# Optimization experiments

Hardware: AMD Instinct MI355X
Metric: run time of the kernel (lower is better)

Reference implementation:

```python
import jax, jax.numpy as jnp
import numpy as np

H = 384  # LSTM hidden size


def _conv1d(x, w, b, stride):
    # x: [B, T, Cin], w: [K, Cin, Cout] (flax 'SAME' padding, channels-last)
    y = jax.lax.conv_general_dilated(
        x, w, window_strides=(stride,), padding='SAME',
        dimension_numbers=('NWC', 'WIO', 'NWC'))
    return y + b


def _lstm(x, Wi, Wh, b, reverse):
    # x: [B, T, D]; Wi: [D, 4H] (input proj, no bias in flax LSTMCell input dense),
    # Wh: [H, 4H] (recurrent proj), b: [4H]. Gate order: i, f, g, o.
    if reverse:
        x = x[:, ::-1]
    B = x.shape[0]
    # precompute all input-to-gate projections in one big GEMM: [B, T, 4H]
    xg = jnp.einsum('btd,dh->bth', x, Wi)

    def step(carry, xg_t):
        c, h = carry
        z = xg_t + h @ Wh + b                      # [B, 4H]
        i, f, g, o = jnp.split(z, 4, axis=-1)
        i = jax.nn.sigmoid(i)
        f = jax.nn.sigmoid(f)
        g = jnp.tanh(g)
        o = jax.nn.sigmoid(o)
        c = f * c + i * g
        h = o * jnp.tanh(c)
        return (c, h), h

    init = (jnp.zeros((B, H), x.dtype), jnp.zeros((B, H), x.dtype))
    _, hs = jax.lax.scan(step, init, jnp.swapaxes(xg, 0, 1))  # hs: [T, B, H]
    hs = jnp.swapaxes(hs, 0, 1)
    if reverse:  # keep_order=True: flip output back to original time order
        hs = hs[:, ::-1]
    return hs


def setup_inputs() -> dict:
    key = jax.random.key(0)
    ks = jax.random.split(key, 12)
    s = 0.05
    B, T = 128, 8000
    return {
        'x': jax.random.normal(ks[0], (B, T, 1), jnp.float32),
        'conv1_w': jax.random.normal(ks[1], (5, 1, 4), jnp.float32) * s,
        'conv1_b': jnp.zeros((4,), jnp.float32),
        'conv2_w': jax.random.normal(ks[2], (5, 4, 16), jnp.float32) * s,
        'conv2_b': jnp.zeros((16,), jnp.float32),
        'conv3_w': jax.random.normal(ks[3], (19, 16, H), jnp.float32) * s,
        'conv3_b': jnp.zeros((H,), jnp.float32),
        'lstm_Wi': jax.random.normal(ks[4], (5, H, 4 * H), jnp.float32) * s,
        'lstm_Wh': jax.random.normal(ks[5], (5, H, 4 * H), jnp.float32) * s,
        'lstm_b': jnp.zeros((5, 4 * H), jnp.float32),
        'dense_w': jax.random.normal(ks[6], (H, 5), jnp.float32) * s,
        'dense_b': jnp.zeros((5,), jnp.float32),
    }


def reference(x, conv1_w, conv1_b, conv2_w, conv2_b, conv3_w, conv3_b,
              lstm_Wi, lstm_Wh, lstm_b, dense_w, dense_b):
    # CNN feature extractor
    x = jax.nn.silu(_conv1d(x, conv1_w, conv1_b, 1))
    x = jax.nn.silu(_conv1d(x, conv2_w, conv2_b, 1))
    x = jax.nn.silu(_conv1d(x, conv3_w, conv3_b, 5))   # [B, T/5, 384]
    # 5 stacked LSTMs, layers 1,3,5 reversed (keep_order), layers 2,4 forward
    for i in range(5):
        x = _lstm(x, lstm_Wi[i], lstm_Wh[i], lstm_b[i], reverse=(i % 2 == 0))
    # CTC head
    return x @ dense_w + dense_b                       # [B, T/5, 5]
```

## Files before the change

### kernel.cpp

```cpp
#include <hip/hip_runtime.h>
#include <math.h>

#define B_SZ 128
#define T_IN 8000
#define T_OUT 1600
#define HDIM 384
#define GDIM 1536
#define TC 40
#define NCHUNK (T_OUT / TC)
#define NTILES (12 * (B_SZ * TC / 128))
#define NLB 64

typedef _Float16 f16;
typedef __attribute__((ext_vector_type(2))) _Float16 f16x2;
typedef __attribute__((ext_vector_type(4))) _Float16 f16x4;
typedef __attribute__((ext_vector_type(8))) _Float16 f16x8;
typedef __attribute__((ext_vector_type(4))) float f32x4;
typedef __attribute__((ext_vector_type(4))) unsigned int u32x4;

__device__ inline float fdot2(f16x2 a, f16x2 b, float c) {
#if __has_builtin(__builtin_amdgcn_fdot2)
  return __builtin_amdgcn_fdot2(a, b, c, false);
#else
  return fmaf((float)a[0], (float)b[0], fmaf((float)a[1], (float)b[1], c));
#endif
}

__device__ inline float rcp_fast(float x) {
#if __has_builtin(__builtin_amdgcn_rcpf)
  return __builtin_amdgcn_rcpf(x);
#else
  return 1.f / x;
#endif
}
__device__ inline float sigf(float z) { return rcp_fast(1.f + __expf(-z)); }
__device__ inline float tanh_fast(float z) {
  z = fminf(fmaxf(z, -15.f), 15.f);
  float e = __expf(2.f * z);
  return (e - 1.f) * rcp_fast(e + 1.f);
}

__global__ __launch_bounds__(256) void conv12_kernel(
    const float* __restrict__ x, const float* __restrict__ w1, const float* __restrict__ b1,
    const float* __restrict__ w2, const float* __restrict__ b2, f16* __restrict__ y2) {
  __shared__ float sw1[20], sb1[4], sw2[320], sb2[16];
  int tid = threadIdx.x;
  if (tid < 20) sw1[tid] = w1[tid];
  if (tid < 4)  sb1[tid] = b1[tid];
  if (tid < 16) sb2[tid] = b2[tid];
  for (int i = tid; i < 320; i += 256) sw2[i] = w2[i];
  __syncthreads();
  int flat = blockIdx.x * 256 + tid;
  int b = flat / T_IN, t = flat % T_IN;
  const float* xb = x + (size_t)b * T_IN;
  float xv[9];
#pragma unroll
  for (int d = 0; d < 9; ++d) {
    int tt = t + d - 4;
    xv[d] = (tt >= 0 && tt < T_IN) ? xb[tt] : 0.f;
  }
  float y1[5][4];
#pragma unroll
  for (int u = 0; u < 5; ++u) {
    int tau = t + u - 2;
    bool valid = (tau >= 0 && tau < T_IN);
#pragma unroll
    for (int co = 0; co < 4; ++co) {
      float a = sb1[co];
#pragma unroll
      for (int k = 0; k < 5; ++k) a = fmaf(xv[u + k], sw1[k * 4 + co], a);
      y1[u][co] = valid ? (a / (1.f + expf(-a))) : 0.f;
    }
  }
  f16x8 o0, o1;
#pragma unroll
  for (int co = 0; co < 16; ++co) {
    float a = sb2[co];
#pragma unroll
    for (int u = 0; u < 5; ++u)
#pragma unroll
      for (int ci = 0; ci < 4; ++ci)
        a = fmaf(y1[u][ci], sw2[(u * 4 + ci) * 16 + co], a);
    float sv = a / (1.f + expf(-a));
    if (co < 8) o0[co] = (f16)sv; else o1[co - 8] = (f16)sv;
  }
  f16x8* dst = (f16x8*)(y2 + (size_t)flat * 16);
  dst[0] = o0;
  dst[1] = o1;
}

__global__ __launch_bounds__(256) void w3cvt_kernel(
    const float* __restrict__ w3, f16* __restrict__ w3t) {
  int idx = blockIdx.x * 256 + threadIdx.x;
  int c = idx / 320, k = idx - c * 320;
  w3t[idx] = (k < 304) ? (f16)w3[(size_t)k * 384 + c] : (f16)0.f;
}

#define C3M 32
#define C3K 320
#define INSP 24
#define BSTP 40

__global__ __launch_bounds__(384) void conv3_kernel(
    const f16* __restrict__ y2, const f16* __restrict__ w3t,
    const float* __restrict__ b3, f16* __restrict__ act) {
  __shared__ f16 in_s[176 * INSP];
  __shared__ f16 bs_t[384 * BSTP];
  int tid = threadIdx.x;
  int b = blockIdx.y;
  int t0 = blockIdx.x * C3M;
  int base_t = t0 * 5 - 7;
  for (int j = tid; j < 352; j += 384) {
    int tau = j >> 1, ci0 = (j & 1) * 8;
    int tt = base_t + tau;
    f16x8 v = {};
    if (tt >= 0 && tt < T_IN)
      v = *(const f16x8*)(y2 + ((size_t)b * T_IN + tt) * 16 + ci0);
    *(f16x8*)&in_s[tau * INSP + ci0] = v;
  }
  int wv = tid >> 6;
  int l = tid & 63;
  int lm = l & 15;
  int lk = l >> 4;
  f32x4 acc[2][4];
#pragma unroll
  for (int mt = 0; mt < 2; ++mt)
#pragma unroll
    for (int q = 0; q < 4; ++q) acc[mt][q] = (f32x4){0.f, 0.f, 0.f, 0.f};
  for (int ks = 0; ks < 10; ++ks) {
    __syncthreads();
    for (int u = tid; u < 1536; u += 384) {
      int c = u >> 2, k8 = u & 3;
      *(f16x8*)&bs_t[c * BSTP + k8 * 8] =
          *(const f16x8*)(w3t + (size_t)c * C3K + ks * 32 + k8 * 8);
    }
    __syncthreads();
    int kg = ks * 32 + lk * 8;
    int kk = kg >> 4, ci = kg & 15;
    f16x8 a0 = *(const f16x8*)&in_s[(lm * 5 + kk) * INSP + ci];
    f16x8 a1 = *(const f16x8*)&in_s[((lm + 16) * 5 + kk) * INSP + ci];
#pragma unroll
    for (int q = 0; q < 4; ++q) {
      f16x8 bf = *(const f16x8*)&bs_t[((wv * 4 + q) * 16 + lm) * BSTP + lk * 8];
      acc[0][q] = __builtin_amdgcn_mfma_f32_16x16x32_f16(a0, bf, acc[0][q], 0, 0, 0);
      acc[1][q] = __builtin_amdgcn_mfma_f32_16x16x32_f16(a1, bf, acc[1][q], 0, 0, 0);
    }
  }
#pragma unroll
  for (int mt = 0; mt < 2; ++mt)
#pragma unroll
    for (int q = 0; q < 4; ++q) {
      int n = (wv * 4 + q) * 16 + lm;
      float bv = b3[n];
#pragma unroll
      for (int r = 0; r < 4; ++r) {
        int m = mt * 16 + lk * 4 + r;
        float a = acc[mt][q][r] + bv;
        a = a / (1.f + expf(-a));
        act[((size_t)b * T_OUT + t0 + m) * HDIM + n] = (f16)a;
      }
    }
}

__global__ __launch_bounds__(256) void whcvt_kernel(
    const float* __restrict__ Wh, f16x2* __restrict__ whB) {
  size_t idx = (size_t)blockIdx.x * 256 + threadIdx.x;
  int d = (int)(idx & 3);
  size_t r1 = idx >> 2;
  int lane = (int)(r1 & 63);
  size_t r2 = r1 >> 6;
  int ks = (int)(r2 % 12);
  size_t r3 = r2 / 12;
  int nt = (int)(r3 % 12);
  size_t r4 = r3 / 12;
  int isl = (int)(r4 & 7);
  int L = (int)(r4 >> 3);
  int cz = nt * 16 + (lane & 15);
  int gate = cz & 3;
  int jj = cz >> 2;
  int gcol = gate * 384 + isl * 48 + jj;
  int k2d = ks * 16 + (lane >> 4) * 4 + d;
  const float* src = Wh + ((size_t)L * 384 + 2 * k2d) * 1536 + gcol;
  f16x2 v;
  v[0] = (f16)src[0];
  v[1] = (f16)src[1536];
  whB[idx] = v;
}

__global__ __launch_bounds__(256) void gemm_xg_kernel(
    const f16* __restrict__ act, const float* __restrict__ Bw,
    f16* __restrict__ C, int lo) {
  __shared__ f16x2 As2[8 * 136];
  __shared__ f16x2 Bs2[8 * 128];
  int tid = threadIdx.x;
  int n0 = blockIdx.x * 128;
  int m0 = blockIdx.y * 128;
  int am = tid >> 2;
  int ak = (tid & 3) * 4;
  int bk = tid >> 5;
  int bn = (tid & 31) * 4;
  int row0 = m0 + am, row1 = row0 + 64;
  const f16* Ap0 = act + ((size_t)(row0 / TC) * T_OUT + lo + row0 % TC) * HDIM + ak;
  const f16* Ap1 = act + ((size_t)(row1 / TC) * T_OUT + lo + row1 % TC) * HDIM + ak;
  const float* Bp = Bw + (size_t)(2 * bk) * GDIM + n0 + bn;
  f16x4 ra0 = *(const f16x4*)Ap0;
  f16x4 ra1 = *(const f16x4*)Ap1;
  float4 rb0 = *(const float4*)Bp;
  float4 rb1 = *(const float4*)(Bp + (size_t)GDIM);
  float acc[8][8];
#pragma unroll
  for (int i = 0; i < 8; ++i)
#pragma unroll
    for (int j = 0; j < 8; ++j) acc[i][j] = 0.f;
  int tx = tid & 15, ty = tid >> 4;
  for (int kt = 0; kt < 24; ++kt) {
    int ak2 = ak >> 1;
    As2[(ak2 + 0) * 136 + am] = (f16x2){ra0[0], ra0[1]};
    As2[(ak2 + 1) * 136 + am] = (f16x2){ra0[2], ra0[3]};
    As2[(ak2 + 0) * 136 + am + 64] = (f16x2){ra1[0], ra1[1]};
    As2[(ak2 + 1) * 136 + am + 64] = (f16x2){ra1[2], ra1[3]};
    Bs2[bk * 128 + bn + 0] = (f16x2){(f16)rb0.x, (f16)rb1.x};
    Bs2[bk * 128 + bn + 1] = (f16x2){(f16)rb0.y, (f16)rb1.y};
    Bs2[bk * 128 + bn + 2] = (f16x2){(f16)rb0.z, (f16)rb1.z};
    Bs2[bk * 128 + bn + 3] = (f16x2){(f16)rb0.w, (f16)rb1.w};
    __syncthreads();
    if (kt < 23) {
      Ap0 += 16; Ap1 += 16; Bp += (size_t)16 * GDIM;
      ra0 = *(const f16x4*)Ap0;
      ra1 = *(const f16x4*)Ap1;
      rb0 = *(const float4*)Bp;
      rb1 = *(const float4*)(Bp + (size_t)GDIM);
    }
#pragma unroll
    for (int k2 = 0; k2 < 8; ++k2) {
      f16x8 a0 = *(const f16x8*)&As2[k2 * 136 + ty * 4];
      f16x8 a1 = *(const f16x8*)&As2[k2 * 136 + 64 + ty * 4];
      f16x8 b0 = *(const f16x8*)&Bs2[k2 * 128 + tx * 4];
      f16x8 b1 = *(const f16x8*)&Bs2[k2 * 128 + 64 + tx * 4];
      f16x2 av[8], bv[8];
#pragma unroll
      for (int q = 0; q < 4; ++q) {
        av[q] = (f16x2){a0[2 * q], a0[2 * q + 1]};
        av[q + 4] = (f16x2){a1[2 * q], a1[2 * q + 1]};
        bv[q] = (f16x2){b0[2 * q], b0[2 * q + 1]};
        bv[q + 4] = (f16x2){b1[2 * q], b1[2 * q + 1]};
      }
#pragma unroll
      for (int i = 0; i < 8; ++i)
#pragma unroll
        for (int j = 0; j < 8; ++j) acc[i][j] = fdot2(av[i], bv[j], acc[i][j]);
    }
    __syncthreads();
  }
#pragma unroll
  for (int i = 0; i < 8; ++i) {
    int mi = (i < 4) ? (ty * 4 + i) : (64 + ty * 4 + i - 4);
    f16* Cp = C + (size_t)(m0 + mi) * GDIM + n0;
    f16x4 p0, p1;
    p0[0] = (f16)acc[i][0]; p0[1] = (f16)acc[i][1]; p0[2] = (f16)acc[i][2]; p0[3] = (f16)acc[i][3];
    p1[0] = (f16)acc[i][4]; p1[1] = (f16)acc[i][5]; p1[2] = (f16)acc[i][6]; p1[3] = (f16)acc[i][7];
    *(f16x4*)(Cp + tx * 4) = p0;
    *(f16x4*)(Cp + 64 + tx * 4) = p1;
  }
}

#define HSTR 784

union FusedSh {
  struct { char h2s[16 * HSTR]; unsigned pub[16 * 25]; } L;
  struct { f16x2 As2[3][8 * 136]; f16x2 Bs2[3][8 * 128]; } G;
  char pad[25600];
};

__global__ __launch_bounds__(768, 1) void fused_kernel(
    const f16* __restrict__ xgc_rd, f16* __restrict__ xgc_wr,
    const f16* __restrict__ whB, const float* __restrict__ bias,
    f16* __restrict__ act, float* __restrict__ cst, const float* __restrict__ Wi,
    unsigned* __restrict__ xh,
    int lo_l, int lo_g, int reverse, int first, int do_gemm, int epoch) {
  __shared__ FusedSh sh;
  int tid = threadIdx.x;

  if (blockIdx.x < NLB) {
    int wid = blockIdx.x;
    int g = wid & 7;
    int isl = wid >> 3;
    int b0 = g * 16;
    int nt = tid >> 6;
    int l = tid & 63;
    int bg = l >> 4;
    int qj = (l >> 2) & 3;
    int gate = l & 3;
    int jj = nt * 4 + qj;
    int hcol = isl * 48 + jj;
    int gcol = gate * 384 + isl * 48 + jj;

    f16x8 wreg[12];
    {
      const f16x8* wp = (const f16x8*)whB + (size_t)(isl * 12 + nt) * 12 * 64 + l;
#pragma unroll
      for (int ks = 0; ks < 12; ++ks) wreg[ks] = wp[(size_t)ks * 64];
#pragma unroll
      for (int ks = 0; ks < 12; ++ks) asm volatile("" : "+v"(wreg[ks]));
    }
    float bias_own = bias[gcol];

    float c_reg[4];
    if (first) {
#pragma unroll
      for (int r = 0; r < 4; ++r) c_reg[r] = 0.f;
      for (int i = tid; i < 16 * HSTR / 16; i += 768)
        *(f16x8*)(sh.L.h2s + i * 16) = (f16x8){};
    } else {
      int tprev = reverse ? (lo_l + TC) : (lo_l - 1);
#pragma unroll
      for (int r = 0; r < 4; ++r)
        c_reg[r] = cst[(size_t)(b0 + bg * 4 + r) * HDIM + hcol];
      int flat = tid * 8;
      int bt = flat / 384, c0 = flat % 384;
      *(f16x8*)(sh.L.h2s + bt * HSTR + c0 * 2) =
          *(const f16x8*)(act + ((size_t)(b0 + bt) * T_OUT + tprev) * HDIM + c0);
    }
    __syncthreads();

    const char* arow = sh.L.h2s + (l & 15) * HSTR + (l >> 4) * 16;
    unsigned short* pubh = (unsigned short*)sh.L.pub;

    int k2 = (tid % 3 == 0) ? (768 + tid / 3) : -1;

    float xv[4];
    {
      int tl0 = reverse ? (TC - 1) : 0;
      const f16* xb = xgc_rd + ((size_t)(b0 + bg * 4) * TC + tl0) * GDIM + gcol;
#pragma unroll
      for (int r = 0; r < 4; ++r) xv[r] = (float)xb[(size_t)r * TC * GDIM];
    }

    for (int s = 0; s < TC; ++s) {
      int t = reverse ? (lo_l + TC - 1 - s) : (lo_l + s);

      f32x4 acc = {0.f, 0.f, 0.f, 0.f};
#pragma unroll
      for (int ks = 0; ks < 12; ++ks) {
        f16x8 a = *(const f16x8*)(arow + ks * 64);
        acc = __builtin_amdgcn_mfma_f32_16x16x32_f16(a, wreg[ks], acc, 0, 0, 0);
      }

      f16 h16[4];
#pragma unroll
      for (int r = 0; r < 4; ++r) {
        float a = acc[r] + xv[r] + bias_own;
        float b = __shfl_xor(a, 1);
        float cc = __shfl_xor(a, 2);
        float dd = __shfl_xor(b, 2);
        float zi = (gate == 0) ? a : (gate == 1) ? b : (gate == 2) ? cc : dd;
        float zf = (gate == 1) ? a : (gate == 0) ? b : (gate == 3) ? cc : dd;
        float zg = (gate == 2) ? a : (gate == 3) ? b : (gate == 0) ? cc : dd;
        float zo = (gate == 3) ? a : (gate == 2) ? b : (gate == 1) ? cc : dd;
        float ig = sigf(zi), fg = sigf(zf), gv = tanh_fast(zg), og = sigf(zo);
        c_reg[r] = fg * c_reg[r] + ig * gv;
        h16[r] = (f16)(og * tanh_fast(c_reg[r]));
      }

      if (s + 1 < TC) {
        unsigned tag = (unsigned)(epoch * TC + s + 1);
        unsigned* slotbase = xh + (size_t)(s & 1) * 128 * 256;

        if (gate == 0) {
          int lcol = nt * 4 + qj;
#pragma unroll
          for (int r = 0; r < 4; ++r)
            pubh[(bg * 4 + r) * 50 + lcol] = __builtin_bit_cast(unsigned short, h16[r]);
        }
        __syncthreads();

        if (tid < 128) {
          int bt = tid >> 3, u = tid & 7;
          const unsigned* pw = sh.L.pub + bt * 25 + u * 3;
          u32x4 dnew;
          dnew[0] = pw[0]; dnew[1] = pw[1]; dnew[2] = pw[2]; dnew[3] = tag;
          u32x4* dp = (u32x4*)(slotbase + (((size_t)(b0 + bt) * 64) + isl * 8 + u) * 4);
          asm volatile("global_store_dwordx4 %0, %1, off sc0 sc1"
                       :: "v"(dp), "v"(dnew) : "memory");
        }

        if (gate == 0) {
#pragma unroll
          for (int r = 0; r < 4; ++r)
            act[((size_t)(b0 + bg * 4 + r) * T_OUT + t) * HDIM + hcol] = h16[r];
        }
        {
          int tl_n = reverse ? (TC - 2 - s) : (s + 1);
          const f16* xb = xgc_rd + ((size_t)(b0 + bg * 4) * TC + tl_n) * GDIM + gcol;
#pragma unroll
          for (int r = 0; r < 4; ++r) xv[r] = (float)xb[(size_t)r * TC * GDIM];
        }

        const u32x4* upA = nullptr; const u32x4* upB = nullptr;
        unsigned* dstA = nullptr; unsigned* dstB = nullptr;
#pragma unroll
        for (int uu = 0; uu < 2; ++uu) {
          int k = (uu == 0) ? tid : k2;
          if (uu == 1 && k < 0) break;
          int bt = k >> 6, rem = k & 63;
          int isl_src = rem >> 3, u = rem & 7;
          unsigned* dst = (unsigned*)(sh.L.h2s + bt * HSTR + isl_src * 96 + u * 12);
          if (isl_src == isl) {
            const unsigned* pw = sh.L.pub + bt * 25 + u * 3;
            dst[0] = pw[0]; dst[1] = pw[1]; dst[2] = pw[2];
          } else {
            const u32x4* up = (const u32x4*)(slotbase + (((size_t)(b0 + bt) * 64) + rem) * 4);
            if (!upA) { upA = up; dstA = dst; } else { upB = up; dstB = dst; }
          }
        }
        if (upA && !upB) {
          u32x4 v;
          while (true) {
            asm volatile("global_load_dwordx4 %0, %1, off sc0 sc1\n\ts_waitcnt vmcnt(0)"
                         : "=v"(v) : "v"(upA) : "memory");
            if (v[3] >= tag) break;
            __builtin_amdgcn_s_sleep(1);
          }
          dstA[0] = v[0]; dstA[1] = v[1]; dstA[2] = v[2];
        } else if (upA && upB) {
          u32x4 v0, v1;
          while (true) {
            asm volatile("global_load_dwordx4 %0, %2, off sc0 sc1\n\t"
                         "global_load_dwordx4 %1, %3, off sc0 sc1\n\t"
                         "s_waitcnt vmcnt(0)"
                         : "=&v"(v0), "=&v"(v1) : "v"(upA), "v"(upB) : "memory");
            if (v0[3] >= tag && v1[3] >= tag) break;
            __builtin_amdgcn_s_sleep(1);
          }
          dstA[0] = v0[0]; dstA[1] = v0[1]; dstA[2] = v0[2];
          dstB[0] = v1[0]; dstB[1] = v1[1]; dstB[2] = v1[2];
        }
        __syncthreads();
      } else {
        if (gate == 0) {
#pragma unroll
          for (int r = 0; r < 4; ++r)
            act[((size_t)(b0 + bg * 4 + r) * T_OUT + t) * HDIM + hcol] = h16[r];
        }
      }
    }
    if (gate == 0) {
#pragma unroll
      for (int r = 0; r < 4; ++r)
        cst[(size_t)(b0 + bg * 4 + r) * HDIM + hcol] = c_reg[r];
    }
  } else {
    if (!do_gemm) return;
    int wid = blockIdx.x - NLB;
    int sub = tid >> 8;
    int stid = tid & 255;
    int tileid = wid + 192 * sub;
    bool valid = (tileid < NTILES);
    int tclamp = valid ? tileid : 0;
    int n0 = (tclamp % 12) * 128;
    int m0 = (tclamp / 12) * 128;
    f16x2* As2 = &sh.G.As2[sub][0];
    f16x2* Bs2 = &sh.G.Bs2[sub][0];
    int am = stid >> 2;
    int ak = (stid & 3) * 4;
    int bk = stid >> 5;
    int bn = (stid & 31) * 4;
    int row0 = m0 + am, row1 = row0 + 64;
    const f16* Ap0 = act + ((size_t)(row0 / TC) * T_OUT + lo_g + row0 % TC) * HDIM + ak;
    const f16* Ap1 = act + ((size_t)(row1 / TC) * T_OUT + lo_g + row1 % TC) * HDIM + ak;
    const float* Bp = Wi + (size_t)(2 * bk) * GDIM + n0 + bn;
    f16x4 ra0 = {}, ra1 = {};
    float4 rb0 = {}, rb1 = {};
    if (valid) {
      ra0 = *(const f16x4*)Ap0;
      ra1 = *(const f16x4*)Ap1;
      rb0 = *(const float4*)Bp;
      rb1 = *(const float4*)(Bp + (size_t)GDIM);
    }
    float acc[8][8];
#pragma unroll
    for (int i = 0; i < 8; ++i)
#pragma unroll
      for (int j = 0; j < 8; ++j) acc[i][j] = 0.f;
    int tx = stid & 15, ty = stid >> 4;
    for (int kt = 0; kt < 24; ++kt) {
      if (valid) {
        int ak2 = ak >> 1;
        As2[(ak2 + 0) * 136 + am] = (f16x2){ra0[0], ra0[1]};
        As2[(ak2 + 1) * 136 + am] = (f16x2){ra0[2], ra0[3]};
        As2[(ak2 + 0) * 136 + am + 64] = (f16x2){ra1[0], ra1[1]};
        As2[(ak2 + 1) * 136 + am + 64] = (f16x2){ra1[2], ra1[3]};
        Bs2[bk * 128 + bn + 0] = (f16x2){(f16)rb0.x, (f16)rb1.x};
        Bs2[bk * 128 + bn + 1] = (f16x2){(f16)rb0.y, (f16)rb1.y};
        Bs2[bk * 128 + bn + 2] = (f16x2){(f16)rb0.z, (f16)rb1.z};
        Bs2[bk * 128 + bn + 3] = (f16x2){(f16)rb0.w, (f16)rb1.w};
      }
      __syncthreads();
      if (valid) {
        if (kt < 23) {
          Ap0 += 16; Ap1 += 16; Bp += (size_t)16 * GDIM;
          ra0 = *(const f16x4*)Ap0;
          ra1 = *(const f16x4*)Ap1;
          rb0 = *(const float4*)Bp;
          rb1 = *(const float4*)(Bp + (size_t)GDIM);
        }
#pragma unroll
        for (int k2i = 0; k2i < 8; ++k2i) {
          f16x8 a0 = *(const f16x8*)&As2[k2i * 136 + ty * 4];
          f16x8 a1 = *(const f16x8*)&As2[k2i * 136 + 64 + ty * 4];
          f16x8 b0 = *(const f16x8*)&Bs2[k2i * 128 + tx * 4];
          f16x8 b1 = *(const f16x8*)&Bs2[k2i * 128 + 64 + tx * 4];
          f16x2 av[8], bv[8];
#pragma unroll
          for (int qq = 0; qq < 4; ++qq) {
            av[qq] = (f16x2){a0[2 * qq], a0[2 * qq + 1]};
            av[qq + 4] = (f16x2){a1[2 * qq], a1[2 * qq + 1]};
            bv[qq] = (f16x2){b0[2 * qq], b0[2 * qq + 1]};
            bv[qq + 4] = (f16x2){b1[2 * qq], b1[2 * qq + 1]};
          }
#pragma unroll
          for (int i = 0; i < 8; ++i)
#pragma unroll
            for (int j = 0; j < 8; ++j) acc[i][j] = fdot2(av[i], bv[j], acc[i][j]);
        }
      }
      __syncthreads();
    }
    if (valid) {
#pragma unroll
      for (int i = 0; i < 8; ++i) {
        int mi = (i < 4) ? (ty * 4 + i) : (64 + ty * 4 + i - 4);
        f16* Cp = xgc_wr + (size_t)(m0 + mi) * GDIM + n0;
        f16x4 p0, p1;
        p0[0] = (f16)acc[i][0]; p0[1] = (f16)acc[i][1]; p0[2] = (f16)acc[i][2]; p0[3] = (f16)acc[i][3];
        p1[0] = (f16)acc[i][4]; p1[1] = (f16)acc[i][5]; p1[2] = (f16)acc[i][6]; p1[3] = (f16)acc[i][7];
        *(f16x4*)(Cp + tx * 4) = p0;
        *(f16x4*)(Cp + 64 + tx * 4) = p1;
      }
    }
  }
}

__global__ __launch_bounds__(256) void dense_kernel(
    const f16* __restrict__ h, const float* __restrict__ dw,
    const float* __restrict__ db, float* __restrict__ out) {
  __shared__ float ws_[1920];
  __shared__ float bs[5];
  int tid = threadIdx.x;
  for (int i = tid; i < 1920; i += 256) ws_[i] = dw[i];
  if (tid < 5) bs[tid] = db[tid];
  __syncthreads();
  size_t flat = (size_t)blockIdx.x * 256 + tid;
  const f16* hp = h + flat * HDIM;
  float acc[5];
#pragma unroll
  for (int o = 0; o < 5; ++o) acc[o] = bs[o];
  for (int d = 0; d < HDIM; d += 4) {
    f16x4 hv = *(const f16x4*)(hp + d);
#pragma unroll
    for (int o = 0; o < 5; ++o) {
      acc[o] = fmaf((float)hv[0], ws_[(d + 0) * 5 + o], acc[o]);
      acc[o] = fmaf((float)hv[1], ws_[(d + 1) * 5 + o], acc[o]);
      acc[o] = fmaf((float)hv[2], ws_[(d + 2) * 5 + o], acc[o]);
      acc[o] = fmaf((float)hv[3], ws_[(d + 3) * 5 + o], acc[o]);
    }
  }
  float* op = out + flat * 5;
#pragma unroll
  for (int o = 0; o < 5; ++o) op[o] = acc[o];
}

extern "C" void kernel_launch(void* const* d_in, const int* in_sizes, int n_in,
                              void* d_out, int out_size, void* d_ws, size_t ws_size,
                              hipStream_t stream) {
  const float* x  = (const float*)d_in[0];
  const float* w1 = (const float*)d_in[1];
  const float* b1 = (const float*)d_in[2];
  const float* w2 = (const float*)d_in[3];
  const float* b2 = (const float*)d_in[4];
  const float* w3 = (const float*)d_in[5];
  const float* b3 = (const float*)d_in[6];
  const float* Wi = (const float*)d_in[7];
  const float* Wh = (const float*)d_in[8];
  const float* lb = (const float*)d_in[9];
  const float* dw = (const float*)d_in[10];
  const float* db = (const float*)d_in[11];
  float* out = (float*)d_out;
  char* ws = (char*)d_ws;

  const size_t ACT_BYTES = (size_t)B_SZ * T_OUT * HDIM * 2;
  const size_t XGC_BYTES = (size_t)B_SZ * TC * GDIM * 2;
  const size_t WHB_BYTES = (size_t)5 * 8 * 12 * 12 * 64 * 16;
  const size_t CST_BYTES = (size_t)B_SZ * HDIM * 4;
  const size_t XH_BYTES  = (size_t)2 * 128 * 64 * 16;
  const size_t W3T_BYTES = (size_t)384 * 320 * 2;
  f16*      act  = (f16*)ws;
  f16*      xgcA = (f16*)(ws + ACT_BYTES);
  f16*      xgcB = (f16*)(ws + ACT_BYTES + XGC_BYTES);
  f16*      whB  = (f16*)(ws + ACT_BYTES + 2 * XGC_BYTES);
  float*    cst  = (float*)(ws + ACT_BYTES + 2 * XGC_BYTES + WHB_BYTES);
  unsigned* xh   = (unsigned*)(ws + ACT_BYTES + 2 * XGC_BYTES + WHB_BYTES + CST_BYTES);
  f16*      w3t  = (f16*)(ws + ACT_BYTES + 2 * XGC_BYTES + WHB_BYTES + CST_BYTES + XH_BYTES);
  f16* y2 = xgcA;

  hipMemsetAsync(xh, 0, XH_BYTES, stream);

  hipLaunchKernelGGL(conv12_kernel, dim3(B_SZ * T_IN / 256), dim3(256), 0, stream,
                     x, w1, b1, w2, b2, y2);
  hipLaunchKernelGGL(w3cvt_kernel, dim3(384 * 320 / 256), dim3(256), 0, stream,
                     w3, w3t);
  hipLaunchKernelGGL(conv3_kernel, dim3(T_OUT / C3M, B_SZ), dim3(384), 0, stream,
                     y2, w3t, b3, act);
  hipLaunchKernelGGL(whcvt_kernel, dim3((unsigned)(WHB_BYTES / 4 / 256)), dim3(256), 0, stream,
                     Wh, (f16x2*)whB);

  for (int l = 0; l < 5; ++l) {
    int rev = (l % 2 == 0) ? 1 : 0;
    const float* wi_p = Wi + (size_t)l * HDIM * GDIM;
    const f16* wh_p = whB + (size_t)l * 8 * 12 * 12 * 64 * 8;
    const float* lb_p = lb + (size_t)l * GDIM;
    int lo0 = rev ? (T_OUT - TC) : 0;
    hipLaunchKernelGGL(gemm_xg_kernel, dim3(GDIM / 128, (B_SZ * TC) / 128), dim3(256), 0, stream,
                       act, wi_p, xgcA, lo0);
    for (int ci = 0; ci < NCHUNK; ++ci) {
      int lo_l = rev ? (T_OUT - (ci + 1) * TC) : (ci * TC);
      int do_gemm = (ci + 1 < NCHUNK) ? 1 : 0;
      int lo_g = do_gemm ? (rev ? (T_OUT - (ci + 2) * TC) : ((ci + 1) * TC)) : 0;
      f16* rd = (ci % 2 == 0) ? xgcA : xgcB;
      f16* wr = (ci % 2 == 0) ? xgcB : xgcA;
      int epoch = l * NCHUNK + ci;
      hipLaunchKernelGGL(fused_kernel, dim3(256), dim3(768), 0, stream,
                         rd, wr, wh_p, lb_p, act, cst, wi_p, xh,
                         lo_l, lo_g, rev, (ci == 0) ? 1 : 0, do_gemm, epoch);
    }
  }
  hipLaunchKernelGGL(dense_kernel, dim3((B_SZ * T_OUT) / 256), dim3(256), 0, stream,
                     act, dw, db, out);
}
```

Before: 26.47 ms.

## Repartition LSTM recurrent blocks into 16 batch groups by 4 hidden slices

```diff
diff --git a/kernel.cpp b/kernel.cpp
--- a/kernel.cpp
+++ b/kernel.cpp
@@ -171,14 +171,14 @@
   size_t r2 = r1 >> 6;
   int ks = (int)(r2 % 12);
   size_t r3 = r2 / 12;
-  int nt = (int)(r3 % 12);
-  size_t r4 = r3 / 12;
-  int isl = (int)(r4 & 7);
-  int L = (int)(r4 >> 3);
+  int nt = (int)(r3 % 24);
+  size_t r4 = r3 / 24;
+  int isl = (int)(r4 & 3);
+  int L = (int)(r4 >> 2);
   int cz = nt * 16 + (lane & 15);
   int gate = cz & 3;
   int jj = cz >> 2;
-  int gcol = gate * 384 + isl * 48 + jj;
+  int gcol = gate * 384 + isl * 96 + jj;
   int k2d = ks * 16 + (lane >> 4) * 4 + d;
   const float* src = Wh + ((size_t)L * 384 + 2 * k2d) * 1536 + gcol;
   f16x2 v;
@@ -283,171 +283,193 @@
 
   if (blockIdx.x < NLB) {
     int wid = blockIdx.x;
-    int g = wid & 7;
-    int isl = wid >> 3;
-    int b0 = g * 16;
-    int nt = tid >> 6;
+    int g = wid & 15;
+    int isl = wid >> 4;
+    int b0 = g * 8;
+    int w = tid >> 6;
     int l = tid & 63;
-    int bg = l >> 4;
+    int lk = l >> 4;
     int qj = (l >> 2) & 3;
     int gate = l & 3;
-    int jj = nt * 4 + qj;
-    int hcol = isl * 48 + jj;
-    int gcol = gate * 384 + isl * 48 + jj;
-
-    f16x8 wreg[12];
+    int jj0 = w * 8 + qj;
+    int hcol0 = isl * 96 + jj0;
+    int gcol0 = gate * 384 + hcol0;
+    int bq = (lk & 1) * 4;
+
+    f16x8 wreg[2][12];
     {
-      const f16x8* wp = (const f16x8*)whB + (size_t)(isl * 12 + nt) * 12 * 64 + l;
-#pragma unroll
-      for (int ks = 0; ks < 12; ++ks) wreg[ks] = wp[(size_t)ks * 64];
-#pragma unroll
-      for (int ks = 0; ks < 12; ++ks) asm volatile("" : "+v"(wreg[ks]));
-    }
-    float bias_own = bias[gcol];
-
-    float c_reg[4];
+      const f16x8* wp = (const f16x8*)whB + (size_t)(isl * 24 + 2 * w) * 12 * 64 + l;
+#pragma unroll
+      for (int ks = 0; ks < 12; ++ks) {
+        wreg[0][ks] = wp[(size_t)ks * 64];
+        wreg[1][ks] = wp[(size_t)(12 + ks) * 64];
+      }
+#pragma unroll
+      for (int ks = 0; ks < 12; ++ks) {
+        asm volatile("" : "+v"(wreg[0][ks]));
+        asm volatile("" : "+v"(wreg[1][ks]));
+      }
+    }
+    float bias0 = bias[gcol0];
+    float bias1 = bias[gcol0 + 4];
+
+    float c0[4], c1[4];
     if (first) {
 #pragma unroll
-      for (int r = 0; r < 4; ++r) c_reg[r] = 0.f;
-      for (int i = tid; i < 16 * HSTR / 16; i += 768)
+      for (int r = 0; r < 4; ++r) { c0[r] = 0.f; c1[r] = 0.f; }
+      for (int i = tid; i < 784; i += 768)
         *(f16x8*)(sh.L.h2s + i * 16) = (f16x8){};
     } else {
       int tprev = reverse ? (lo_l + TC) : (lo_l - 1);
 #pragma unroll
-      for (int r = 0; r < 4; ++r)
-        c_reg[r] = cst[(size_t)(b0 + bg * 4 + r) * HDIM + hcol];
-      int flat = tid * 8;
-      int bt = flat / 384, c0 = flat % 384;
-      *(f16x8*)(sh.L.h2s + bt * HSTR + c0 * 2) =
-          *(const f16x8*)(act + ((size_t)(b0 + bt) * T_OUT + tprev) * HDIM + c0);
+      for (int r = 0; r < 4; ++r) {
+        c0[r] = cst[(size_t)(b0 + bq + r) * HDIM + hcol0];
+        c1[r] = cst[(size_t)(b0 + bq + r) * HDIM + hcol0 + 4];
+      }
+      int flat = tid * 4;
+      int bt = flat / 384, cc0 = flat % 384;
+      *(f16x4*)(sh.L.h2s + bt * HSTR + cc0 * 2) =
+          *(const f16x4*)(act + ((size_t)(b0 + bt) * T_OUT + tprev) * HDIM + cc0);
+      if (tid < 392) {
+        int row = 8 + tid / 49, off = (tid % 49) * 16;
+        *(f16x8*)(sh.L.h2s + row * HSTR + off) = (f16x8){};
+      }
     }
     __syncthreads();
 
-    const char* arow = sh.L.h2s + (l & 15) * HSTR + (l >> 4) * 16;
+    const char* arow = sh.L.h2s + (l & 15) * HSTR + lk * 16;
     unsigned short* pubh = (unsigned short*)sh.L.pub;
 
-    int k2 = (tid % 3 == 0) ? (768 + tid / 3) : -1;
-
-    float xv[4];
+    float xv0[4], xv1[4];
     {
       int tl0 = reverse ? (TC - 1) : 0;
-      const f16* xb = xgc_rd + ((size_t)(b0 + bg * 4) * TC + tl0) * GDIM + gcol;
-#pragma unroll
-      for (int r = 0; r < 4; ++r) xv[r] = (float)xb[(size_t)r * TC * GDIM];
+      const f16* xb = xgc_rd + ((size_t)(b0 + bq) * TC + tl0) * GDIM + gcol0;
+#pragma unroll
+      for (int r = 0; r < 4; ++r) {
+        xv0[r] = (float)xb[(size_t)r * TC * GDIM];
+        xv1[r] = (float)xb[(size_t)r * TC * GDIM + 4];
+      }
     }
 
     for (int s = 0; s < TC; ++s) {
       int t = reverse ? (lo_l + TC - 1 - s) : (lo_l + s);
 
-      f32x4 acc = {0.f, 0.f, 0.f, 0.f};
+      f32x4 acc0 = {0.f, 0.f, 0.f, 0.f};
+      f32x4 acc1 = {0.f, 0.f, 0.f, 0.f};
 #pragma unroll
       for (int ks = 0; ks < 12; ++ks) {
         f16x8 a = *(const f16x8*)(arow + ks * 64);
-        acc = __builtin_amdgcn_mfma_f32_16x16x32_f16(a, wreg[ks], acc, 0, 0, 0);
-      }
-
-      f16 h16[4];
+        acc0 = __builtin_amdgcn_mfma_f32_16x16x32_f16(a, wreg[0][ks], acc0, 0, 0, 0);
+        acc1 = __builtin_amdgcn_mfma_f32_16x16x32_f16(a, wreg[1][ks], acc1, 0, 0, 0);
+      }
+
+      f16 h0[4], h1[4];
 #pragma unroll
       for (int r = 0; r < 4; ++r) {
-        float a = acc[r] + xv[r] + bias_own;
-        float b = __shfl_xor(a, 1);
-        float cc = __shfl_xor(a, 2);
-        float dd = __shfl_xor(b, 2);
-        float zi = (gate == 0) ? a : (gate == 1) ? b : (gate == 2) ? cc : dd;
-        float zf = (gate == 1) ? a : (gate == 0) ? b : (gate == 3) ? cc : dd;
-        float zg = (gate == 2) ? a : (gate == 3) ? b : (gate == 0) ? cc : dd;
-        float zo = (gate == 3) ? a : (gate == 2) ? b : (gate == 1) ? cc : dd;
-        float ig = sigf(zi), fg = sigf(zf), gv = tanh_fast(zg), og = sigf(zo);
-        c_reg[r] = fg * c_reg[r] + ig * gv;
-        h16[r] = (f16)(og * tanh_fast(c_reg[r]));
+        {
+          float a = acc0[r] + xv0[r] + bias0;
+          float b = __shfl_xor(a, 1);
+          float cc = __shfl_xor(a, 2);
+          float dd = __shfl_xor(b, 2);
+          float zi = (gate == 0) ? a : (gate == 1) ? b : (gate == 2) ? cc : dd;
+          float zf = (gate == 1) ? a : (gate == 0) ? b : (gate == 3) ? cc : dd;
+          float zg = (gate == 2) ? a : (gate == 3) ? b : (gate == 0) ? cc : dd;
+          float zo = (gate == 3) ? a : (gate == 2) ? b : (gate == 1) ? cc : dd;
+          float ig = sigf(zi), fg = sigf(zf), gv = tanh_fast(zg), og = sigf(zo);
+          c0[r] = fg * c0[r] + ig * gv;
+          h0[r] = (f16)(og * tanh_fast(c0[r]));
+        }
+        {
+          float a = acc1[r] + xv1[r] + bias1;
+          float b = __shfl_xor(a, 1);
+          float cc = __shfl_xor(a, 2);
+          float dd = __shfl_xor(b, 2);
+          float zi = (gate == 0) ? a : (gate == 1) ? b : (gate == 2) ? cc : dd;
+          float zf = (gate == 1) ? a : (gate == 0) ? b : (gate == 3) ? cc : dd;
+          float zg = (gate == 2) ? a : (gate == 3) ? b : (gate == 0) ? cc : dd;
+          float zo = (gate == 3) ? a : (gate == 2) ? b : (gate == 1) ? cc : dd;
+          float ig = sigf(zi), fg = sigf(zf), gv = tanh_fast(zg), og = sigf(zo);
+          c1[r] = fg * c1[r] + ig * gv;
+          h1[r] = (f16)(og * tanh_fast(c1[r]));
+        }
       }
 
       if (s + 1 < TC) {
         unsigned tag = (unsigned)(epoch * TC + s + 1);
         unsigned* slotbase = xh + (size_t)(s & 1) * 128 * 256;
 
-        if (gate == 0) {
-          int lcol = nt * 4 + qj;
-#pragma unroll
-          for (int r = 0; r < 4; ++r)
-            pubh[(bg * 4 + r) * 50 + lcol] = __builtin_bit_cast(unsigned short, h16[r]);
+        if (gate == 0 && lk < 2) {
+#pragma unroll
+          for (int r = 0; r < 4; ++r) {
+            pubh[(lk * 4 + r) * 98 + jj0] = __builtin_bit_cast(unsigned short, h0[r]);
+            pubh[(lk * 4 + r) * 98 + jj0 + 4] = __builtin_bit_cast(unsigned short, h1[r]);
+          }
         }
         __syncthreads();
 
         if (tid < 128) {
-          int bt = tid >> 3, u = tid & 7;
-          const unsigned* pw = sh.L.pub + bt * 25 + u * 3;
+          int bt = tid >> 4, u = tid & 15;
+          const unsigned* pw = sh.L.pub + bt * 49 + u * 3;
           u32x4 dnew;
           dnew[0] = pw[0]; dnew[1] = pw[1]; dnew[2] = pw[2]; dnew[3] = tag;
-          u32x4* dp = (u32x4*)(slotbase + (((size_t)(b0 + bt) * 64) + isl * 8 + u) * 4);
+          u32x4* dp = (u32x4*)(slotbase + (((size_t)(b0 + bt) * 64) + isl * 16 + u) * 4);
           asm volatile("global_store_dwordx4 %0, %1, off sc0 sc1"
                        :: "v"(dp), "v"(dnew) : "memory");
         }
 
-        if (gate == 0) {
-#pragma unroll
-          for (int r = 0; r < 4; ++r)
-            act[((size_t)(b0 + bg * 4 + r) * T_OUT + t) * HDIM + hcol] = h16[r];
+        if (gate == 0 && lk < 2) {
+#pragma unroll
+          for (int r = 0; r < 4; ++r) {
+            act[((size_t)(b0 + lk * 4 + r) * T_OUT + t) * HDIM + hcol0] = h0[r];
+            act[((size_t)(b0 + lk * 4 + r) * T_OUT + t) * HDIM + hcol0 + 4] = h1[r];
+          }
         }
         {
           int tl_n = reverse ? (TC - 2 - s) : (s + 1);
-          const f16* xb = xgc_rd + ((size_t)(b0 + bg * 4) * TC + tl_n) * GDIM + gcol;
-#pragma unroll
-          for (int r = 0; r < 4; ++r) xv[r] = (float)xb[(size_t)r * TC * GDIM];
-        }
-
-        const u32x4* upA = nullptr; const u32x4* upB = nullptr;
-        unsigned* dstA = nullptr; unsigned* dstB = nullptr;
-#pragma unroll
-        for (int uu = 0; uu < 2; ++uu) {
-          int k = (uu == 0) ? tid : k2;
-          if (uu == 1 && k < 0) break;
-          int bt = k >> 6, rem = k & 63;
-          int isl_src = rem >> 3, u = rem & 7;
-          unsigned* dst = (unsigned*)(sh.L.h2s + bt * HSTR + isl_src * 96 + u * 12);
+          const f16* xb = xgc_rd + ((size_t)(b0 + bq) * TC + tl_n) * GDIM + gcol0;
+#pragma unroll
+          for (int r = 0; r < 4; ++r) {
+            xv0[r] = (float)xb[(size_t)r * TC * GDIM];
+            xv1[r] = (float)xb[(size_t)r * TC * GDIM + 4];
+          }
+        }
+
+        if (tid < 512) {
+          int bt = tid >> 6, rem = tid & 63;
+          int isl_src = rem >> 4, u = rem & 15;
+          unsigned* dst = (unsigned*)(sh.L.h2s + bt * HSTR + isl_src * 192 + u * 12);
           if (isl_src == isl) {
-            const unsigned* pw = sh.L.pub + bt * 25 + u * 3;
+            const unsigned* pw = sh.L.pub + bt * 49 + u * 3;
             dst[0] = pw[0]; dst[1] = pw[1]; dst[2] = pw[2];
           } else {
             const u32x4* up = (const u32x4*)(slotbase + (((size_t)(b0 + bt) * 64) + rem) * 4);
-            if (!upA) { upA = up; dstA = dst; } else { upB = up; dstB = dst; }
+            u32x4 v;
+            while (true) {
+              asm volatile("global_load_dwordx4 %0, %1, off sc0 sc1\n\ts_waitcnt vmcnt(0)"
+                           : "=v"(v) : "v"(up) : "memory");
+              if (v[3] >= tag) break;
+              __builtin_amdgcn_s_sleep(1);
+            }
+            dst[0] = v[0]; dst[1] = v[1]; dst[2] = v[2];
           }
-        }
-        if (upA && !upB) {
-          u32x4 v;
-          while (true) {
-            asm volatile("global_load_dwordx4 %0, %1, off sc0 sc1\n\ts_waitcnt vmcnt(0)"
-                         : "=v"(v) : "v"(upA) : "memory");
-            if (v[3] >= tag) break;
-            __builtin_amdgcn_s_sleep(1);
-          }
-          dstA[0] = v[0]; dstA[1] = v[1]; dstA[2] = v[2];
-        } else if (upA && upB) {
-          u32x4 v0, v1;
-          while (true) {
-            asm volatile("global_load_dwordx4 %0, %2, off sc0 sc1\n\t"
-                         "global_load_dwordx4 %1, %3, off sc0 sc1\n\t"
-                         "s_waitcnt vmcnt(0)"
-                         : "=&v"(v0), "=&v"(v1) : "v"(upA), "v"(upB) : "memory");
-            if (v0[3] >= tag && v1[3] >= tag) break;
-            __builtin_amdgcn_s_sleep(1);
-          }
-          dstA[0] = v0[0]; dstA[1] = v0[1]; dstA[2] = v0[2];
-          dstB[0] = v1[0]; dstB[1] = v1[1]; dstB[2] = v1[2];
         }
         __syncthreads();
       } else {
-        if (gate == 0) {
-#pragma unroll
-          for (int r = 0; r < 4; ++r)
-            act[((size_t)(b0 + bg * 4 + r) * T_OUT + t) * HDIM + hcol] = h16[r];
-        }
-      }
-    }
-    if (gate == 0) {
-#pragma unroll
-      for (int r = 0; r < 4; ++r)
-        cst[(size_t)(b0 + bg * 4 + r) * HDIM + hcol] = c_reg[r];
+        if (gate == 0 && lk < 2) {
+#pragma unroll
+          for (int r = 0; r < 4; ++r) {
+            act[((size_t)(b0 + lk * 4 + r) * T_OUT + t) * HDIM + hcol0] = h0[r];
+            act[((size_t)(b0 + lk * 4 + r) * T_OUT + t) * HDIM + hcol0 + 4] = h1[r];
+          }
+        }
+      }
+    }
+    if (gate == 0 && lk < 2) {
+#pragma unroll
+      for (int r = 0; r < 4; ++r) {
+        cst[(size_t)(b0 + lk * 4 + r) * HDIM + hcol0] = c0[r];
+        cst[(size_t)(b0 + lk * 4 + r) * HDIM + hcol0 + 4] = c1[r];
+      }
     }
   } else {
     if (!do_gemm) return;
@@ -590,7 +612,7 @@
 
   const size_t ACT_BYTES = (size_t)B_SZ * T_OUT * HDIM * 2;
   const size_t XGC_BYTES = (size_t)B_SZ * TC * GDIM * 2;
-  const size_t WHB_BYTES = (size_t)5 * 8 * 12 * 12 * 64 * 16;
+  const size_t WHB_BYTES = (size_t)5 * 4 * 24 * 12 * 64 * 16;
   const size_t CST_BYTES = (size_t)B_SZ * HDIM * 4;
   const size_t XH_BYTES  = (size_t)2 * 128 * 64 * 16;
   const size_t W3T_BYTES = (size_t)384 * 320 * 2;
@@ -617,7 +639,7 @@
   for (int l = 0; l < 5; ++l) {
     int rev = (l % 2 == 0) ? 1 : 0;
     const float* wi_p = Wi + (size_t)l * HDIM * GDIM;
-    const f16* wh_p = whB + (size_t)l * 8 * 12 * 12 * 64 * 8;
+    const f16* wh_p = whB + (size_t)l * 4 * 24 * 12 * 64 * 8;
     const float* lb_p = lb + (size_t)l * GDIM;
     int lo0 = rev ? (T_OUT - TC) : 0;
     hipLaunchKernelGGL(gemm_xg_kernel, dim3(GDIM / 128, (B_SZ * TC) / 128), dim3(256), 0, stream,
```

Result: slower. 37.30 ms (+40.9%).
